# Kernel tuning notes

Measured on AMD Instinct MI355X. Metric: run time of the kernel, lower is better.

The kernel has to match this reference:

```python
import jax, jax.numpy as jnp
import numpy as np

B, L, V, D, C, R = 8, 2048, 32000, 512, 64, 64
NBLK = 2           # n_layers - 1
H = 2 * D          # stem hidden dim
STD = 0.02


def _ln(x, w, b):
    m = x.mean(-1, keepdims=True)
    v = ((x - m) ** 2).mean(-1, keepdims=True)
    return (x - m) / jnp.sqrt(v + 1e-5) * w + b


def setup_inputs() -> dict:
    key = jax.random.key(0)
    ks = jax.random.split(key, 16)
    n = lambda k, shp: jax.random.normal(k, shp, dtype=jnp.float32) * STD
    return {
        "token_ids": jax.random.randint(ks[0], (B, L), 0, V),
        "tok_emb": n(ks[1], (V, D)),
        "pos_emb": n(ks[2], (L, D)),
        "stem_ln_w": jnp.ones((NBLK, D), jnp.float32),
        "stem_ln_b": jnp.zeros((NBLK, D), jnp.float32),
        "stem_w1": n(ks[3], (NBLK, D, H)),
        "stem_b1": jnp.zeros((NBLK, H), jnp.float32),
        "stem_w2": n(ks[4], (NBLK, H, D)),
        "stem_b2": jnp.zeros((NBLK, D), jnp.float32),
        "role_ln_w": jnp.ones((D,), jnp.float32),
        "role_ln_b": jnp.zeros((D,), jnp.float32),
        "Wa": n(ks[5], (D, R)),
        "Wb": n(ks[6], (D, R)),
        "Wc": n(ks[7], (D, R)),
        "class_a": n(ks[8], (C, R)),
        "class_b": n(ks[9], (C, R)),
        "class_c": n(ks[10], (C, R)),
        "query_ln_w": jnp.ones((D,), jnp.float32),
        "query_ln_b": jnp.zeros((D,), jnp.float32),
        "Wq": n(ks[11], (D, C)),
        "bq": jnp.zeros((C,), jnp.float32),
    }


def reference(token_ids, tok_emb, pos_emb, stem_ln_w, stem_ln_b, stem_w1,
              stem_b1, stem_w2, stem_b2, role_ln_w, role_ln_b, Wa, Wb, Wc,
              class_a, class_b, class_c, query_ln_w, query_ln_b, Wq, bq):
    seq_len = token_ids.shape[1]
    x = tok_emb[token_ids] + pos_emb[:seq_len][None, :, :]  # [B,L,D]
    for i in range(NBLK):
        h = _ln(x, stem_ln_w[i], stem_ln_b[i])
        h = jax.nn.gelu(h @ stem_w1[i] + stem_b1[i], approximate=False)
        x = x + h @ stem_w2[i] + stem_b2[i]
    prefix = _ln(x[:, :-1], role_ln_w, role_ln_b)  # [B,L-1,D]
    a = jnp.tanh(prefix @ Wa)
    b = jnp.tanh(prefix @ Wb)
    c = jnp.tanh(prefix @ Wc)
    ua = jnp.einsum('blr,cr->blc', a, class_a)  # [B,L-1,C]
    ub = jnp.einsum('blr,cr->blc', b, class_b)
    uc = jnp.einsum('blr,cr->blc', c, class_c)
    # exact ordered-triplet sum  sum_{i<j<k} ua_i * ub_j * uc_k  via exclusive cumsums
    prefA = jnp.cumsum(ua, axis=1) - ua            # sum_{i<j} ua_i
    t = ub * prefA
    prefT = jnp.cumsum(t, axis=1) - t              # sum_{j<k} ub_j * prefA_j
    s = (uc * prefT).sum(axis=1)                   # [B,C]
    Lp = max(seq_len - 1, 1)
    denom = max(Lp * (Lp - 1) * (Lp - 2) / 6.0, 1.0)
    q = _ln(x[:, -1], query_ln_w, query_ln_b)
    return s / denom + q @ Wq + bq
```

## Files before the change

kernel.cpp:

```cpp
#include <hip/hip_runtime.h>

#define NROWS 16384
#define LSEQ  2048
#define NB    8

typedef short v8s __attribute__((ext_vector_type(8)));
typedef float v4f __attribute__((ext_vector_type(4)));

__device__ __forceinline__ unsigned short f2bf(float f) {
    unsigned int u = __float_as_uint(f);
    return (unsigned short)((u + 0x7fffu + ((u >> 16) & 1u)) >> 16);
}
__device__ __forceinline__ float bf2f(unsigned short u) {
    return __uint_as_float(((unsigned int)u) << 16);
}

__device__ __forceinline__ float fast_gelu(float v) {
    float z = fabsf(v) * 0.70710678118654752f;
    float t = __builtin_amdgcn_rcpf(1.0f + 0.3275911f * z);
    float poly = t * (0.254829592f + t * (-0.284496736f + t * (1.421413741f +
                 t * (-1.453152027f + t * 1.061405429f))));
    float erfz = 1.0f - poly * __expf(-z * z);
    float er = copysignf(erfz, v);
    return 0.5f * v * (1.0f + er);
}
__device__ __forceinline__ float fast_tanh(float y) {
    float e = __expf(2.0f * y);
    return (e - 1.0f) * __builtin_amdgcn_rcpf(e + 1.0f);
}

__global__ __launch_bounds__(256) void prep_kernel(
        const float* __restrict__ w1, const float* __restrict__ w2,
        const float* __restrict__ wa, const float* __restrict__ wb, const float* __restrict__ wc,
        const float* __restrict__ ca, const float* __restrict__ cb, const float* __restrict__ cc,
        unsigned short* __restrict__ w1T, unsigned short* __restrict__ w2T,
        unsigned short* __restrict__ wabcT, unsigned short* __restrict__ clsb) {
    int id = blockIdx.x;
    int tx = threadIdx.x, ty = threadIdx.y;
    if (id < 2144) {
        const float* in; unsigned short* out; int R, C, bx, by, ldo;
        if (id < 1024) {
            int l = id >> 9, r = id & 511;
            in = w1 + l * 524288; out = w1T + l * 524288;
            R = 512; C = 1024; bx = r & 31; by = r >> 5; ldo = 512;
        } else if (id < 2048) {
            int l = (id - 1024) >> 9, r = (id - 1024) & 511;
            in = w2 + l * 524288; out = w2T + l * 524288;
            R = 1024; C = 512; bx = r & 15; by = r >> 4; ldo = 1024;
        } else {
            int g = (id - 2048) >> 5, r = (id - 2048) & 31;
            in = (g == 0) ? wa : (g == 1) ? wb : wc;
            out = wabcT + g * 32768;
            R = 512; C = 64; bx = r & 1; by = r >> 1; ldo = 512;
        }
        __shared__ unsigned short tile[32][33];
        int c0 = bx * 32, r0 = by * 32;
        for (int i = ty; i < 32; i += 8) {
            int r = r0 + i, c = c0 + tx;
            tile[i][tx] = (r < R && c < C) ? f2bf(in[(size_t)r * C + c]) : (unsigned short)0;
        }
        __syncthreads();
        for (int i = ty; i < 32; i += 8) {
            int c = c0 + i, r = r0 + tx;
            if (r < R && c < C) out[(size_t)c * ldo + r] = tile[tx][i];
        }
    } else {
        int g = id - 2144;
        const float* src = (g == 0) ? ca : (g == 1) ? cb : cc;
        unsigned short* dst = clsb + g * 4096;
        int tid = ty * 32 + tx;
        for (int i = tid; i < 4096; i += 256) dst[i] = f2bf(src[i]);
    }
}

__global__ __launch_bounds__(256) void embed_ln_kernel(const int* __restrict__ ids,
        const float* __restrict__ tok, const float* __restrict__ pos,
        const float* __restrict__ g, const float* __restrict__ b,
        unsigned short* __restrict__ x, unsigned short* __restrict__ hl) {
    int row = blockIdx.x;
    int l = row & (LSEQ - 1);
    int t = threadIdx.x;
    int id = ids[row];
    float2 tv = *(const float2*)(tok + (size_t)id * 512 + 2 * t);
    float2 pv = *(const float2*)(pos + (size_t)l * 512 + 2 * t);
    float a0 = tv.x + pv.x, a1 = tv.y + pv.y;
    unsigned int xp = (unsigned int)f2bf(a0) | ((unsigned int)f2bf(a1) << 16);
    *(unsigned int*)(x + (size_t)row * 512 + 2 * t) = xp;
    float s = a0 + a1, s2 = a0 * a0 + a1 * a1;
    #pragma unroll
    for (int o = 32; o > 0; o >>= 1) { s += __shfl_down(s, o); s2 += __shfl_down(s2, o); }
    __shared__ float ps[4], ps2[4], mv[2];
    int w = t >> 6;
    if ((t & 63) == 0) { ps[w] = s; ps2[w] = s2; }
    __syncthreads();
    if (t == 0) {
        float S = ps[0] + ps[1] + ps[2] + ps[3];
        float S2 = ps2[0] + ps2[1] + ps2[2] + ps2[3];
        float m = S * (1.0f / 512.0f);
        float var = S2 * (1.0f / 512.0f) - m * m;
        mv[0] = m; mv[1] = 1.0f / sqrtf(var + 1e-5f);
    }
    __syncthreads();
    float m = mv[0], r = mv[1];
    unsigned int hp = (unsigned int)f2bf((a0 - m) * r * g[2 * t] + b[2 * t])
                    | ((unsigned int)f2bf((a1 - m) * r * g[2 * t + 1] + b[2 * t + 1]) << 16);
    *(unsigned int*)(hl + (size_t)row * 512 + 2 * t) = hp;
}

__global__ __launch_bounds__(256) void ln_kernel(const unsigned short* __restrict__ x,
        const float* __restrict__ g, const float* __restrict__ b,
        unsigned short* __restrict__ out) {
    int row = blockIdx.x;
    int t = threadIdx.x;
    unsigned int xp = *(const unsigned int*)(x + (size_t)row * 512 + 2 * t);
    float a0 = bf2f((unsigned short)(xp & 0xffff)), a1 = bf2f((unsigned short)(xp >> 16));
    float s = a0 + a1, s2 = a0 * a0 + a1 * a1;
    #pragma unroll
    for (int o = 32; o > 0; o >>= 1) { s += __shfl_down(s, o); s2 += __shfl_down(s2, o); }
    __shared__ float ps[4], ps2[4], mv[2];
    int w = t >> 6;
    if ((t & 63) == 0) { ps[w] = s; ps2[w] = s2; }
    __syncthreads();
    if (t == 0) {
        float S = ps[0] + ps[1] + ps[2] + ps[3];
        float S2 = ps2[0] + ps2[1] + ps2[2] + ps2[3];
        float m = S * (1.0f / 512.0f);
        float var = S2 * (1.0f / 512.0f) - m * m;
        mv[0] = m; mv[1] = 1.0f / sqrtf(var + 1e-5f);
    }
    __syncthreads();
    float m = mv[0], r = mv[1];
    unsigned int hp = (unsigned int)f2bf((a0 - m) * r * g[2 * t] + b[2 * t])
                    | ((unsigned int)f2bf((a1 - m) * r * g[2 * t + 1] + b[2 * t + 1]) << 16);
    *(unsigned int*)(out + (size_t)row * 512 + 2 * t) = hp;
}

#define EPI_GELU_BF16  0
#define EPI_RES_BF16   1

template <int EPI, int TN>
__global__ __launch_bounds__(256) void gemm_r2(
        const unsigned short* __restrict__ A, int lda,
        const unsigned short* __restrict__ BT, int ldb,
        const float* __restrict__ bias,
        const unsigned short* __restrict__ xres,
        unsigned short* __restrict__ Cout, int ldc, int K) {
    constexpr int NJ = TN / 32;
    __shared__ unsigned short As[128][40] __attribute__((aligned(16)));
    __shared__ unsigned short Bs[TN][40] __attribute__((aligned(16)));
    const int t = threadIdx.x;
    const int lane = t & 63, wave = t >> 6;
    const int quad = lane >> 4, l16 = lane & 15;
    const int wm = (wave >> 1) * 64, wn = (wave & 1) * (TN / 2);
    const long tileM = (long)blockIdx.x * 128, tileN = (long)blockIdx.y * TN;
    const int arow = t >> 2, acol = (t & 3) * 8;

    const unsigned short* gA0 = A + (tileM + arow) * lda + acol;
    const unsigned short* gA1 = gA0 + 64 * (long)lda;
    const unsigned short* gB0 = BT + (tileN + arow) * ldb + acol;
    const unsigned short* gB1 = gB0 + 64 * (long)ldb;

    v4f acc[4][NJ] = {};
    uint4 a0, a1, b0, b1;

    a0 = *(const uint4*)gA0; a1 = *(const uint4*)gA1; gA0 += 32; gA1 += 32;
    b0 = *(const uint4*)gB0; gB0 += 32;
    if (TN == 128) { b1 = *(const uint4*)gB1; gB1 += 32; }
    *(uint4*)&As[arow][acol] = a0;
    *(uint4*)&As[arow + 64][acol] = a1;
    *(uint4*)&Bs[arow][acol] = b0;
    if (TN == 128) *(uint4*)&Bs[arow + 64][acol] = b1;

    const int nk = K >> 5;
    for (int kk = 0; kk < nk; ++kk) {
        __syncthreads();
        const bool more = kk + 1 < nk;
        if (more) {
            a0 = *(const uint4*)gA0; a1 = *(const uint4*)gA1; gA0 += 32; gA1 += 32;
            b0 = *(const uint4*)gB0; gB0 += 32;
            if (TN == 128) { b1 = *(const uint4*)gB1; gB1 += 32; }
        }
        v8s af[4], bfr[NJ];
        #pragma unroll
        for (int i = 0; i < 4; ++i) af[i] = *(const v8s*)&As[wm + i * 16 + l16][quad * 8];
        #pragma unroll
        for (int j = 0; j < NJ; ++j) bfr[j] = *(const v8s*)&Bs[wn + j * 16 + l16][quad * 8];
        #pragma unroll
        for (int i = 0; i < 4; ++i)
            #pragma unroll
            for (int j = 0; j < NJ; ++j)
                acc[i][j] = __builtin_amdgcn_mfma_f32_16x16x32_bf16(af[i], bfr[j], acc[i][j], 0, 0, 0);
        __syncthreads();
        if (more) {
            *(uint4*)&As[arow][acol] = a0;
            *(uint4*)&As[arow + 64][acol] = a1;
            *(uint4*)&Bs[arow][acol] = b0;
            if (TN == 128) *(uint4*)&Bs[arow + 64][acol] = b1;
        }
    }

    #pragma unroll
    for (int i = 0; i < 4; ++i) {
        #pragma unroll
        for (int j = 0; j < NJ; ++j) {
            long col = tileN + wn + j * 16 + l16;
            #pragma unroll
            for (int r = 0; r < 4; ++r) {
                long row = tileM + wm + i * 16 + quad * 4 + r;
                float v = acc[i][j][r];
                if (EPI == EPI_GELU_BF16) {
                    v = fast_gelu(v + bias[col]);
                    Cout[row * ldc + col] = f2bf(v);
                } else {
                    v += bias[col] + bf2f(xres[row * ldc + col]);
                    Cout[row * ldc + col] = f2bf(v);
                }
            }
        }
    }
}

__global__ __launch_bounds__(256) void tanh_class_kernel(
        const unsigned short* __restrict__ A,
        const unsigned short* __restrict__ WT,
        const unsigned short* __restrict__ cls,
        unsigned short* __restrict__ uu) {
    __shared__ unsigned short As[2][128 * 32] __attribute__((aligned(16)));
    __shared__ unsigned short Bs[2][64 * 32] __attribute__((aligned(16)));
    __shared__ unsigned short P[128 * 72] __attribute__((aligned(16)));
    const int t = threadIdx.x;
    const int lane = t & 63, wave = t >> 6;
    const int quad = lane >> 4, l16 = lane & 15;
    const int wm = (wave >> 1) * 64, wn = (wave & 1) * 32;
    const long tileM = (long)blockIdx.x * 128;
    const int g = blockIdx.y;

    const int srow = t >> 2, scg = t & 3;
    const int spos = scg ^ ((srow >> 1) & 3);
    const int swz = quad ^ ((l16 >> 1) & 3);
    const int uoff = srow * 32 + spos * 8;

    const unsigned short* BT = WT + g * 32768;
    v8s cf[2][2];
    #pragma unroll
    for (int ks = 0; ks < 2; ++ks)
        #pragma unroll
        for (int j = 0; j < 2; ++j)
            cf[ks][j] = *(const v8s*)&cls[g * 4096 + (wn + j * 16 + l16) * 64 + ks * 32 + quad * 8];

    const unsigned short* gA0 = A + (tileM + srow) * 512 + scg * 8;
    const unsigned short* gA1 = gA0 + 64 * 512;
    const unsigned short* gB0 = BT + srow * 512 + scg * 8;

    v4f acc[4][2] = {};
    uint4 a0, a1, b0;
    a0 = *(const uint4*)gA0; a1 = *(const uint4*)gA1; gA0 += 32; gA1 += 32;
    b0 = *(const uint4*)gB0; gB0 += 32;
    *(uint4*)&As[0][uoff] = a0;
    *(uint4*)&As[0][uoff + 64 * 32] = a1;
    *(uint4*)&Bs[0][uoff] = b0;

    for (int kk = 0; kk < 16; ++kk) {
        const int p = kk & 1;
        const bool more = kk < 15;
        if (more) {
            a0 = *(const uint4*)gA0; a1 = *(const uint4*)gA1; gA0 += 32; gA1 += 32;
            b0 = *(const uint4*)gB0; gB0 += 32;
        }
        __syncthreads();
        v8s af[4], bfr[2];
        #pragma unroll
        for (int i = 0; i < 4; ++i) af[i] = *(const v8s*)&As[p][(wm + i * 16 + l16) * 32 + swz * 8];
        #pragma unroll
        for (int j = 0; j < 2; ++j) bfr[j] = *(const v8s*)&Bs[p][(wn + j * 16 + l16) * 32 + swz * 8];
        #pragma unroll
        for (int i = 0; i < 4; ++i)
            #pragma unroll
            for (int j = 0; j < 2; ++j)
                acc[i][j] = __builtin_amdgcn_mfma_f32_16x16x32_bf16(af[i], bfr[j], acc[i][j], 0, 0, 0);
        if (more) {
            *(uint4*)&As[1 - p][uoff] = a0;
            *(uint4*)&As[1 - p][uoff + 64 * 32] = a1;
            *(uint4*)&Bs[1 - p][uoff] = b0;
        }
    }

    #pragma unroll
    for (int i = 0; i < 4; ++i)
        #pragma unroll
        for (int j = 0; j < 2; ++j)
            #pragma unroll
            for (int r = 0; r < 4; ++r)
                P[(wm + i * 16 + quad * 4 + r) * 72 + wn + j * 16 + l16] = f2bf(fast_tanh(acc[i][j][r]));
    __syncthreads();

    v4f acc2[4][2] = {};
    #pragma unroll
    for (int ks = 0; ks < 2; ++ks) {
        v8s paf[4];
        #pragma unroll
        for (int i = 0; i < 4; ++i)
            paf[i] = *(const v8s*)&P[(wm + i * 16 + l16) * 72 + ks * 32 + quad * 8];
        #pragma unroll
        for (int i = 0; i < 4; ++i)
            #pragma unroll
            for (int j = 0; j < 2; ++j)
                acc2[i][j] = __builtin_amdgcn_mfma_f32_16x16x32_bf16(paf[i], cf[ks][j], acc2[i][j], 0, 0, 0);
    }

    #pragma unroll
    for (int i = 0; i < 4; ++i)
        #pragma unroll
        for (int j = 0; j < 2; ++j) {
            int col = wn + j * 16 + l16;
            #pragma unroll
            for (int r = 0; r < 4; ++r) {
                long row = tileM + wm + i * 16 + quad * 4 + r;
                uu[row * 192 + g * 64 + col] = f2bf(acc2[i][j][r]);
            }
        }
}

__global__ __launch_bounds__(64) void scan_part_kernel(const unsigned short* __restrict__ u,
                                                       float* __restrict__ part) {
    int b = blockIdx.x, seg = blockIdx.y;
    int c = threadIdx.x;
    int l0 = seg * 32;
    int l1 = l0 + 32; if (l1 > 2047) l1 = 2047;
    float sA = 0.f, sB = 0.f, sC = 0.f, T = 0.f, M = 0.f, U = 0.f;
    const unsigned short* base = u + ((size_t)b * LSEQ + l0) * 192 + c;
    for (int l = l0; l < l1; ++l) {
        float ua = bf2f(base[0]), ub = bf2f(base[64]), uc = bf2f(base[128]);
        base += 192;
        U += uc * T;
        M += uc * sB;
        T += ub * sA;
        sA += ua; sB += ub; sC += uc;
    }
    float* p = part + ((size_t)(b * 64 + seg)) * 384 + c;
    p[0] = sA; p[64] = sB; p[128] = sC; p[192] = T; p[256] = M; p[320] = U;
}

__global__ __launch_bounds__(64) void scan_combine_kernel(const float* __restrict__ part,
                                                          float* __restrict__ s) {
    int b = blockIdx.x;
    int c = threadIdx.x;
    const float* p = part + (size_t)b * 64 * 384 + c;
    float A = p[0], B = p[64], Tt = p[192], Mt = p[256], Ut = p[320];
    for (int seg = 1; seg < 64; ++seg) {
        const float* q = p + seg * 384;
        float a2 = q[0], b2 = q[64], c2 = q[128], t2 = q[192], m2 = q[256], u2 = q[320];
        float Un = Ut + u2 + c2 * Tt + A * m2;
        float Tn = Tt + t2 + A * b2;
        float Mn = Mt + m2 + B * c2;
        A += a2; B += b2;
        Ut = Un; Tt = Tn; Mt = Mn;
    }
    s[b * 64 + c] = Ut;
}

__global__ __launch_bounds__(64) void final_kernel(const unsigned short* __restrict__ x,
        const float* __restrict__ s,
        const float* __restrict__ qw, const float* __restrict__ qb,
        const float* __restrict__ Wq, const float* __restrict__ bq,
        float* __restrict__ out, float inv_denom) {
    int b = blockIdx.x;
    int c = threadIdx.x;
    __shared__ float q[512];
    __shared__ float mv[2];
    const unsigned short* xr = x + ((size_t)b * LSEQ + (LSEQ - 1)) * 512;
    float s1 = 0.f, s2 = 0.f;
    for (int i = c; i < 512; i += 64) { float v = bf2f(xr[i]); q[i] = v; s1 += v; s2 += v * v; }
    #pragma unroll
    for (int o = 32; o > 0; o >>= 1) { s1 += __shfl_down(s1, o); s2 += __shfl_down(s2, o); }
    if (c == 0) {
        float m = s1 * (1.0f / 512.0f);
        float var = s2 * (1.0f / 512.0f) - m * m;
        mv[0] = m; mv[1] = 1.0f / sqrtf(var + 1e-5f);
    }
    __syncthreads();
    float m = mv[0], r = mv[1];
    for (int i = c; i < 512; i += 64) q[i] = (q[i] - m) * r * qw[i] + qb[i];
    __syncthreads();
    float acc = 0.f;
    for (int d = 0; d < 512; ++d) acc += q[d] * Wq[d * 64 + c];
    out[b * 64 + c] = s[b * 64 + c] * inv_denom + acc + bq[c];
}

extern "C" void kernel_launch(void* const* d_in, const int* in_sizes, int n_in,
                              void* d_out, int out_size, void* d_ws, size_t ws_size,
                              hipStream_t stream) {
    const int*   token_ids   = (const int*)d_in[0];
    const float* tok_emb     = (const float*)d_in[1];
    const float* pos_emb     = (const float*)d_in[2];
    const float* stem_ln_w   = (const float*)d_in[3];
    const float* stem_ln_b   = (const float*)d_in[4];
    const float* stem_w1     = (const float*)d_in[5];
    const float* stem_b1     = (const float*)d_in[6];
    const float* stem_w2     = (const float*)d_in[7];
    const float* stem_b2     = (const float*)d_in[8];
    const float* role_ln_w   = (const float*)d_in[9];
    const float* role_ln_b   = (const float*)d_in[10];
    const float* Wa          = (const float*)d_in[11];
    const float* Wb          = (const float*)d_in[12];
    const float* Wc          = (const float*)d_in[13];
    const float* class_a     = (const float*)d_in[14];
    const float* class_b     = (const float*)d_in[15];
    const float* class_c     = (const float*)d_in[16];
    const float* query_ln_w  = (const float*)d_in[17];
    const float* query_ln_b  = (const float*)d_in[18];
    const float* Wq          = (const float*)d_in[19];
    const float* bq          = (const float*)d_in[20];
    float* out = (float*)d_out;

    char* wsb = (char*)d_ws;
    unsigned short* x    = (unsigned short*)(wsb);
    unsigned short* hl   = (unsigned short*)(wsb + 16777216);
    unsigned short* Hb   = (unsigned short*)(wsb + 33554432);
    unsigned short* uu   = (unsigned short*)(wsb + 67108864);
    float* part          = (float*)(wsb + 73400320);
    float* svec          = (float*)(wsb + 74186752);
    unsigned short* w1T  = (unsigned short*)(wsb + 74188800);
    unsigned short* w2T  = (unsigned short*)(wsb + 76285952);
    unsigned short* wabcT= (unsigned short*)(wsb + 78383104);
    unsigned short* clsb = (unsigned short*)(wsb + 78579712);

    prep_kernel<<<2147, dim3(32, 8), 0, stream>>>(stem_w1, stem_w2, Wa, Wb, Wc,
        class_a, class_b, class_c, w1T, w2T, wabcT, clsb);

    embed_ln_kernel<<<NROWS, 256, 0, stream>>>(token_ids, tok_emb, pos_emb,
                                               stem_ln_w, stem_ln_b, x, hl);

    for (int i = 0; i < 2; ++i) {
        if (i > 0)
            ln_kernel<<<NROWS, 256, 0, stream>>>(x, stem_ln_w + 512, stem_ln_b + 512, hl);
        gemm_r2<EPI_GELU_BF16, 128><<<dim3(128, 8), 256, 0, stream>>>(
            hl, 512, w1T + i * 524288, 512, stem_b1 + i * 1024, nullptr, Hb, 1024, 512);
        gemm_r2<EPI_RES_BF16, 64><<<dim3(128, 8), 256, 0, stream>>>(
            Hb, 1024, w2T + i * 524288, 1024, stem_b2 + i * 512, x, x, 512, 1024);
    }

    ln_kernel<<<NROWS, 256, 0, stream>>>(x, role_ln_w, role_ln_b, hl);

    tanh_class_kernel<<<dim3(128, 3), 256, 0, stream>>>(hl, wabcT, clsb, uu);

    scan_part_kernel<<<dim3(NB, 64), 64, 0, stream>>>(uu, part);
    scan_combine_kernel<<<NB, 64, 0, stream>>>(part, svec);

    float inv_denom = (float)(6.0 / (2047.0 * 2046.0 * 2045.0));
    final_kernel<<<NB, 64, 0, stream>>>(x, svec, query_ln_w, query_ln_b, Wq, bq, out, inv_denom);
}
```

Before: 354.8 us.

## Use one wave per row for layernorms and transposed MFMA for vector stores

The embed and layernorm kernels now process one row per wavefront with 8 elements per lane and 16-byte loads and stores. This removes the shared-memory reduction and both block barriers, and cuts the launch grid by four. The GEMM and tanh/class kernels swap the MFMA operand order so each lane holds four consecutive columns of one row. That lets epilogue stores, bias loads and residual loads become 8-byte vectors instead of scattered 2-byte accesses. The change relies on the transposed accumulator layout being mapped correctly in every epilogue.

```diff
diff --git a/kernel.cpp b/kernel.cpp
--- a/kernel.cpp
+++ b/kernel.cpp
@@ -77,62 +77,78 @@
         const float* __restrict__ tok, const float* __restrict__ pos,
         const float* __restrict__ g, const float* __restrict__ b,
         unsigned short* __restrict__ x, unsigned short* __restrict__ hl) {
-    int row = blockIdx.x;
-    int l = row & (LSEQ - 1);
-    int t = threadIdx.x;
+    int wave = threadIdx.x >> 6, lane = threadIdx.x & 63;
+    long row = (long)blockIdx.x * 4 + wave;
+    int l = (int)(row & (LSEQ - 1));
     int id = ids[row];
-    float2 tv = *(const float2*)(tok + (size_t)id * 512 + 2 * t);
-    float2 pv = *(const float2*)(pos + (size_t)l * 512 + 2 * t);
-    float a0 = tv.x + pv.x, a1 = tv.y + pv.y;
-    unsigned int xp = (unsigned int)f2bf(a0) | ((unsigned int)f2bf(a1) << 16);
-    *(unsigned int*)(x + (size_t)row * 512 + 2 * t) = xp;
-    float s = a0 + a1, s2 = a0 * a0 + a1 * a1;
+    int d = lane * 8;
+    float4 t0 = *(const float4*)(tok + (size_t)id * 512 + d);
+    float4 t1 = *(const float4*)(tok + (size_t)id * 512 + d + 4);
+    float4 p0 = *(const float4*)(pos + (size_t)l * 512 + d);
+    float4 p1 = *(const float4*)(pos + (size_t)l * 512 + d + 4);
+    float a[8] = {t0.x + p0.x, t0.y + p0.y, t0.z + p0.z, t0.w + p0.w,
+                  t1.x + p1.x, t1.y + p1.y, t1.z + p1.z, t1.w + p1.w};
+    unsigned int xp[4];
+    #pragma unroll
+    for (int i = 0; i < 4; ++i)
+        xp[i] = (unsigned int)f2bf(a[2 * i]) | ((unsigned int)f2bf(a[2 * i + 1]) << 16);
+    *(uint4*)(x + row * 512 + d) = *(uint4*)xp;
+    float s = 0.f, s2 = 0.f;
+    #pragma unroll
+    for (int i = 0; i < 8; ++i) { s += a[i]; s2 += a[i] * a[i]; }
     #pragma unroll
     for (int o = 32; o > 0; o >>= 1) { s += __shfl_down(s, o); s2 += __shfl_down(s2, o); }
-    __shared__ float ps[4], ps2[4], mv[2];
-    int w = t >> 6;
-    if ((t & 63) == 0) { ps[w] = s; ps2[w] = s2; }
-    __syncthreads();
-    if (t == 0) {
-        float S = ps[0] + ps[1] + ps[2] + ps[3];
-        float S2 = ps2[0] + ps2[1] + ps2[2] + ps2[3];
-        float m = S * (1.0f / 512.0f);
-        float var = S2 * (1.0f / 512.0f) - m * m;
-        mv[0] = m; mv[1] = 1.0f / sqrtf(var + 1e-5f);
-    }
-    __syncthreads();
-    float m = mv[0], r = mv[1];
-    unsigned int hp = (unsigned int)f2bf((a0 - m) * r * g[2 * t] + b[2 * t])
-                    | ((unsigned int)f2bf((a1 - m) * r * g[2 * t + 1] + b[2 * t + 1]) << 16);
-    *(unsigned int*)(hl + (size_t)row * 512 + 2 * t) = hp;
+    s = __shfl(s, 0); s2 = __shfl(s2, 0);
+    float m = s * (1.0f / 512.0f);
+    float rinv = 1.0f / sqrtf(s2 * (1.0f / 512.0f) - m * m + 1e-5f);
+    float4 g0 = *(const float4*)(g + d), g1 = *(const float4*)(g + d + 4);
+    float4 b0 = *(const float4*)(b + d), b1 = *(const float4*)(b + d + 4);
+    float gg[8] = {g0.x, g0.y, g0.z, g0.w, g1.x, g1.y, g1.z, g1.w};
+    float bb[8] = {b0.x, b0.y, b0.z, b0.w, b1.x, b1.y, b1.z, b1.w};
+    unsigned int hp[4];
+    #pragma unroll
+    for (int i = 0; i < 4; ++i) {
+        unsigned short lo = f2bf((a[2 * i]     - m) * rinv * gg[2 * i]     + bb[2 * i]);
+        unsigned short hi = f2bf((a[2 * i + 1] - m) * rinv * gg[2 * i + 1] + bb[2 * i + 1]);
+        hp[i] = (unsigned int)lo | ((unsigned int)hi << 16);
+    }
+    *(uint4*)(hl + row * 512 + d) = *(uint4*)hp;
 }
 
 __global__ __launch_bounds__(256) void ln_kernel(const unsigned short* __restrict__ x,
         const float* __restrict__ g, const float* __restrict__ b,
         unsigned short* __restrict__ out) {
-    int row = blockIdx.x;
-    int t = threadIdx.x;
-    unsigned int xp = *(const unsigned int*)(x + (size_t)row * 512 + 2 * t);
-    float a0 = bf2f((unsigned short)(xp & 0xffff)), a1 = bf2f((unsigned short)(xp >> 16));
-    float s = a0 + a1, s2 = a0 * a0 + a1 * a1;
+    int wave = threadIdx.x >> 6, lane = threadIdx.x & 63;
+    long row = (long)blockIdx.x * 4 + wave;
+    int d = lane * 8;
+    uint4 xp = *(const uint4*)(x + row * 512 + d);
+    const unsigned int* xw = (const unsigned int*)&xp;
+    float a[8];
+    #pragma unroll
+    for (int i = 0; i < 4; ++i) {
+        a[2 * i]     = bf2f((unsigned short)(xw[i] & 0xffff));
+        a[2 * i + 1] = bf2f((unsigned short)(xw[i] >> 16));
+    }
+    float s = 0.f, s2 = 0.f;
+    #pragma unroll
+    for (int i = 0; i < 8; ++i) { s += a[i]; s2 += a[i] * a[i]; }
     #pragma unroll
     for (int o = 32; o > 0; o >>= 1) { s += __shfl_down(s, o); s2 += __shfl_down(s2, o); }
-    __shared__ float ps[4], ps2[4], mv[2];
-    int w = t >> 6;
-    if ((t & 63) == 0) { ps[w] = s; ps2[w] = s2; }
-    __syncthreads();
-    if (t == 0) {
-        float S = ps[0] + ps[1] + ps[2] + ps[3];
-        float S2 = ps2[0] + ps2[1] + ps2[2] + ps2[3];
-        float m = S * (1.0f / 512.0f);
-        float var = S2 * (1.0f / 512.0f) - m * m;
-        mv[0] = m; mv[1] = 1.0f / sqrtf(var + 1e-5f);
-    }
-    __syncthreads();
-    float m = mv[0], r = mv[1];
-    unsigned int hp = (unsigned int)f2bf((a0 - m) * r * g[2 * t] + b[2 * t])
-                    | ((unsigned int)f2bf((a1 - m) * r * g[2 * t + 1] + b[2 * t + 1]) << 16);
-    *(unsigned int*)(out + (size_t)row * 512 + 2 * t) = hp;
+    s = __shfl(s, 0); s2 = __shfl(s2, 0);
+    float m = s * (1.0f / 512.0f);
+    float rinv = 1.0f / sqrtf(s2 * (1.0f / 512.0f) - m * m + 1e-5f);
+    float4 g0 = *(const float4*)(g + d), g1 = *(const float4*)(g + d + 4);
+    float4 b0 = *(const float4*)(b + d), b1 = *(const float4*)(b + d + 4);
+    float gg[8] = {g0.x, g0.y, g0.z, g0.w, g1.x, g1.y, g1.z, g1.w};
+    float bb[8] = {b0.x, b0.y, b0.z, b0.w, b1.x, b1.y, b1.z, b1.w};
+    unsigned int hp[4];
+    #pragma unroll
+    for (int i = 0; i < 4; ++i) {
+        unsigned short lo = f2bf((a[2 * i]     - m) * rinv * gg[2 * i]     + bb[2 * i]);
+        unsigned short hi = f2bf((a[2 * i + 1] - m) * rinv * gg[2 * i + 1] + bb[2 * i + 1]);
+        hp[i] = (unsigned int)lo | ((unsigned int)hi << 16);
+    }
+    *(uint4*)(out + row * 512 + d) = *(uint4*)hp;
 }
 
 #define EPI_GELU_BF16  0
@@ -189,7 +205,7 @@
         for (int i = 0; i < 4; ++i)
             #pragma unroll
             for (int j = 0; j < NJ; ++j)
-                acc[i][j] = __builtin_amdgcn_mfma_f32_16x16x32_bf16(af[i], bfr[j], acc[i][j], 0, 0, 0);
+                acc[i][j] = __builtin_amdgcn_mfma_f32_16x16x32_bf16(bfr[j], af[i], acc[i][j], 0, 0, 0);
         __syncthreads();
         if (more) {
             *(uint4*)&As[arow][acol] = a0;
@@ -201,21 +217,25 @@
 
     #pragma unroll
     for (int i = 0; i < 4; ++i) {
+        long m = tileM + wm + i * 16 + l16;
         #pragma unroll
         for (int j = 0; j < NJ; ++j) {
-            long col = tileN + wn + j * 16 + l16;
-            #pragma unroll
-            for (int r = 0; r < 4; ++r) {
-                long row = tileM + wm + i * 16 + quad * 4 + r;
-                float v = acc[i][j][r];
-                if (EPI == EPI_GELU_BF16) {
-                    v = fast_gelu(v + bias[col]);
-                    Cout[row * ldc + col] = f2bf(v);
-                } else {
-                    v += bias[col] + bf2f(xres[row * ldc + col]);
-                    Cout[row * ldc + col] = f2bf(v);
-                }
+            long n0 = tileN + wn + j * 16 + quad * 4;
+            float4 bi = *(const float4*)&bias[n0];
+            const float* bip = (const float*)&bi;
+            unsigned short pk[4];
+            if (EPI == EPI_GELU_BF16) {
+                #pragma unroll
+                for (int r = 0; r < 4; ++r)
+                    pk[r] = f2bf(fast_gelu(acc[i][j][r] + bip[r]));
+            } else {
+                ushort4 xr4 = *(const ushort4*)&xres[m * ldc + n0];
+                const unsigned short* xp = (const unsigned short*)&xr4;
+                #pragma unroll
+                for (int r = 0; r < 4; ++r)
+                    pk[r] = f2bf(acc[i][j][r] + bip[r] + bf2f(xp[r]));
             }
+            *(ushort4*)&Cout[m * ldc + n0] = *(ushort4*)pk;
         }
     }
 }
@@ -277,7 +297,7 @@
         for (int i = 0; i < 4; ++i)
             #pragma unroll
             for (int j = 0; j < 2; ++j)
-                acc[i][j] = __builtin_amdgcn_mfma_f32_16x16x32_bf16(af[i], bfr[j], acc[i][j], 0, 0, 0);
+                acc[i][j] = __builtin_amdgcn_mfma_f32_16x16x32_bf16(bfr[j], af[i], acc[i][j], 0, 0, 0);
         if (more) {
             *(uint4*)&As[1 - p][uoff] = a0;
             *(uint4*)&As[1 - p][uoff + 64 * 32] = a1;
@@ -286,12 +306,17 @@
     }
 
     #pragma unroll
-    for (int i = 0; i < 4; ++i)
-        #pragma unroll
-        for (int j = 0; j < 2; ++j)
+    for (int i = 0; i < 4; ++i) {
+        int m = wm + i * 16 + l16;
+        #pragma unroll
+        for (int j = 0; j < 2; ++j) {
+            int n0 = wn + j * 16 + quad * 4;
+            unsigned short pk[4];
             #pragma unroll
-            for (int r = 0; r < 4; ++r)
-                P[(wm + i * 16 + quad * 4 + r) * 72 + wn + j * 16 + l16] = f2bf(fast_tanh(acc[i][j][r]));
+            for (int r = 0; r < 4; ++r) pk[r] = f2bf(fast_tanh(acc[i][j][r]));
+            *(ushort4*)&P[m * 72 + n0] = *(ushort4*)pk;
+        }
+    }
     __syncthreads();
 
     v4f acc2[4][2] = {};
@@ -305,20 +330,21 @@
         for (int i = 0; i < 4; ++i)
             #pragma unroll
             for (int j = 0; j < 2; ++j)
-                acc2[i][j] = __builtin_amdgcn_mfma_f32_16x16x32_bf16(paf[i], cf[ks][j], acc2[i][j], 0, 0, 0);
-    }
-
-    #pragma unroll
-    for (int i = 0; i < 4; ++i)
+                acc2[i][j] = __builtin_amdgcn_mfma_f32_16x16x32_bf16(cf[ks][j], paf[i], acc2[i][j], 0, 0, 0);
+    }
+
+    #pragma unroll
+    for (int i = 0; i < 4; ++i) {
+        long m = tileM + wm + i * 16 + l16;
         #pragma unroll
         for (int j = 0; j < 2; ++j) {
-            int col = wn + j * 16 + l16;
+            int c0 = wn + j * 16 + quad * 4;
+            unsigned short pk[4];
             #pragma unroll
-            for (int r = 0; r < 4; ++r) {
-                long row = tileM + wm + i * 16 + quad * 4 + r;
-                uu[row * 192 + g * 64 + col] = f2bf(acc2[i][j][r]);
-            }
-        }
+            for (int r = 0; r < 4; ++r) pk[r] = f2bf(acc2[i][j][r]);
+            *(ushort4*)&uu[m * 192 + g * 64 + c0] = *(ushort4*)pk;
+        }
+    }
 }
 
 __global__ __launch_bounds__(64) void scan_part_kernel(const unsigned short* __restrict__ u,
@@ -428,19 +454,19 @@
     prep_kernel<<<2147, dim3(32, 8), 0, stream>>>(stem_w1, stem_w2, Wa, Wb, Wc,
         class_a, class_b, class_c, w1T, w2T, wabcT, clsb);
 
-    embed_ln_kernel<<<NROWS, 256, 0, stream>>>(token_ids, tok_emb, pos_emb,
-                                               stem_ln_w, stem_ln_b, x, hl);
+    embed_ln_kernel<<<NROWS / 4, 256, 0, stream>>>(token_ids, tok_emb, pos_emb,
+                                                   stem_ln_w, stem_ln_b, x, hl);
 
     for (int i = 0; i < 2; ++i) {
         if (i > 0)
-            ln_kernel<<<NROWS, 256, 0, stream>>>(x, stem_ln_w + 512, stem_ln_b + 512, hl);
+            ln_kernel<<<NROWS / 4, 256, 0, stream>>>(x, stem_ln_w + 512, stem_ln_b + 512, hl);
         gemm_r2<EPI_GELU_BF16, 128><<<dim3(128, 8), 256, 0, stream>>>(
             hl, 512, w1T + i * 524288, 512, stem_b1 + i * 1024, nullptr, Hb, 1024, 512);
         gemm_r2<EPI_RES_BF16, 64><<<dim3(128, 8), 256, 0, stream>>>(
             Hb, 1024, w2T + i * 524288, 1024, stem_b2 + i * 512, x, x, 512, 1024);
     }
 
-    ln_kernel<<<NROWS, 256, 0, stream>>>(x, role_ln_w, role_ln_b, hl);
+    ln_kernel<<<NROWS / 4, 256, 0, stream>>>(x, role_ln_w, role_ln_b, hl);
 
     tanh_class_kernel<<<dim3(128, 3), 256, 0, stream>>>(hl, wabcT, clsb, uu);
 
```

After: 351.0 us. No clear change (-1.1%).
